# Kernel tuning notes

Measured on AMD Instinct MI355X. Metric: run time of the kernel, lower is better.

Reference implementation:

```python
import jax, jax.numpy as jnp
import numpy as np

B, DAYS, N, E = 2, 8, 10000, 80000
C_IN, C_OUT, H = 32, 32, 4
NEG_SLOPE = 0.2


def setup_inputs() -> dict:
    key = jax.random.key(0)
    ks = jax.random.split(key, 7)
    x = jax.random.randint(ks[0], (B, DAYS, N), 0, N)
    adjacency = jax.random.randint(ks[1], (2, E), 0, N)
    embedding = jax.random.normal(ks[2], (N, C_IN), dtype=jnp.float32)
    # GATConv linear: in_channels -> heads*out_channels
    W = jax.random.normal(ks[3], (C_IN, H * C_OUT), dtype=jnp.float32) / np.sqrt(C_IN)
    att_src = jax.random.normal(ks[4], (H, C_OUT), dtype=jnp.float32) / np.sqrt(C_OUT)
    att_dst = jax.random.normal(ks[5], (H, C_OUT), dtype=jnp.float32) / np.sqrt(C_OUT)
    bias = jnp.zeros((H * C_OUT,), dtype=jnp.float32)
    return {"x": x, "adjacency": adjacency, "embedding": embedding,
            "W": W, "att_src": att_src, "att_dst": att_dst, "bias": bias}


def _gat_forward(feat, src, dst, W, att_src, att_dst, bias):
    # feat: [G, N, C_IN]; same edge list shared across the G graphs
    G = feat.shape[0]
    xh = (feat @ W).reshape(G, N, H, C_OUT)              # [G,N,H,C]
    a_src = jnp.einsum('gnhc,hc->gnh', xh, att_src)       # [G,N,H]
    a_dst = jnp.einsum('gnhc,hc->gnh', xh, att_dst)
    alpha = a_src[:, src] + a_dst[:, dst]                 # [G,Et,H]
    alpha = jnp.where(alpha >= 0, alpha, NEG_SLOPE * alpha)

    def per_graph(al, msgs):
        # segment softmax over incoming edges of each dst node
        m = jax.ops.segment_max(al, dst, num_segments=N)  # [N,H]
        e = jnp.exp(al - m[dst])                          # [Et,H]
        s = jax.ops.segment_sum(e, dst, num_segments=N)
        w = e / (s[dst] + 1e-16)
        out = jax.ops.segment_sum(w[..., None] * msgs, dst, num_segments=N)
        return out                                        # [N,H,C]

    out = jax.vmap(per_graph)(alpha, xh[:, src])          # [G,N,H,C]
    return out.reshape(G, N, H * C_OUT) + bias


def reference(x, adjacency, embedding, W, att_src, att_dst, bias):
    Bd, Dd = x.shape[0], x.shape[1]
    feat = embedding[x].reshape(-1, N, C_IN)              # [G,N,C_IN]
    # GATConv default add_self_loops=True
    loops = jnp.arange(N, dtype=adjacency.dtype)
    src = jnp.concatenate([adjacency[0], loops])
    dst = jnp.concatenate([adjacency[1], loops])
    out = _gat_forward(feat, src, dst, W, att_src, att_dst, bias)
    return out.reshape(Bd, Dd, -1)
```

## Files before the change

### kernel.cpp

```cpp
#include <hip/hip_runtime.h>
#include <hip/hip_bf16.h>
#include <math.h>

#define C_IN 32
#define H 4
#define C_OUT 32
#define HC (H * C_OUT)
#define NEG_SLOPE 0.2f
#define CSR_STRIDE 64

typedef float v2f __attribute__((ext_vector_type(2)));

#define RPB 16
__global__ __launch_bounds__(256) void build_kernel(
        const int* __restrict__ adj, int E, int N,
        int* __restrict__ deg, int* __restrict__ csr,
        const float* __restrict__ emb, const float* __restrict__ W,
        const float* __restrict__ att_src, const float* __restrict__ att_dst,
        __hip_bfloat16* __restrict__ T, float* __restrict__ ta_src,
        float* __restrict__ ta_dst, int tblocks) {
    if ((int)blockIdx.x >= tblocks) {
        int e = (blockIdx.x - tblocks) * 256 + threadIdx.x;
        int Et = E + N;
        if (e < Et) {
            int s = (e < E) ? adj[e] : (e - E);
            int d = (e < E) ? adj[E + e] : (e - E);
            int pos = atomicAdd(&deg[d], 1);
            if (pos < CSR_STRIDE) csr[(d << 6) + pos] = s;
        }
        return;
    }
    int t = threadIdx.x;
    int sub = t >> 7;
    int tc = t & 127;
    int h = tc >> 5, c = tc & 31;
    int base = blockIdx.x * RPB;
    int nmax = (N - base < RPB) ? (N - base) : RPB;

    float wcol[C_IN];
#pragma unroll
    for (int k = 0; k < C_IN; k++) wcol[k] = W[k * HC + tc];
    float as = att_src[h * C_OUT + c];
    float adw = att_dst[h * C_OUT + c];

    for (int it = sub; it < nmax; it += 2) {
        int r = __builtin_amdgcn_readfirstlane(base + it);
        const float* ep = emb + (size_t)r * C_IN;
        float acc = 0.f;
#pragma unroll
        for (int k = 0; k < C_IN; k++) acc += ep[k] * wcol[k];
        T[(size_t)r * HC + tc] = __float2bfloat16(acc);
        float ps = acc * as, pd = acc * adw;
#pragma unroll
        for (int o = 16; o; o >>= 1) {
            ps += __shfl_xor(ps, o, 32);
            pd += __shfl_xor(pd, o, 32);
        }
        if (c == 0) {
            ta_src[r * H + h] = ps;
            ta_dst[r * H + h] = pd;
        }
    }
}

__global__ __launch_bounds__(256) void agg_kernel(
        const int* __restrict__ deg, const int* __restrict__ csr,
        const int* __restrict__ x, const uint2* __restrict__ Tu2,
        const float* __restrict__ ta_src, const float* __restrict__ ta_dst,
        const float* __restrict__ bias, float* __restrict__ out, int N, int G) {
    int wid = threadIdx.x >> 6;
    int lane = threadIdx.x & 63;
    int g = blockIdx.y * 4 + wid;
    if (g >= G) return;
    int n = blockIdx.x;

    int half = lane >> 5;
    int q = lane & 31;
    int hq = q >> 3;
    int h16 = lane >> 4;
    int e_sub = lane & 15;
    int widx = (hq << 4) + half;

    int dg = deg[n];
    if (dg > CSR_STRIDE) dg = CSR_STRIDE;
    int cbase = n << 6;
    const int* xg_arr = x + (size_t)g * N;
    int xgn = xg_arr[n];
    float ad = ta_dst[xgn * H + h16];

    float dsum = 0.f;
    v2f a01 = {0.f, 0.f}, a23 = {0.f, 0.f};

    for (int c0 = 0; c0 < dg; c0 += 16) {
        int cnt = dg - c0;
        cnt = (cnt > 16) ? 16 : cnt;
        int xg_e = 0;
        float w_pre = 0.f;
        if (e_sub < cnt) {
            int s = csr[cbase + c0 + e_sub];
            xg_e = xg_arr[s];
            float v = ta_src[xg_e * H + h16] + ad;
            v = (v >= 0.f) ? v : NEG_SLOPE * v;
            w_pre = __expf(v);
        }
        int ntrip = (cnt + 1) >> 1;
#pragma unroll
        for (int i = 0; i < 8; i++) {
            if (i >= ntrip) break;
            float w = __shfl(w_pre, widx + 2 * i, 64);
            int xg = __shfl(xg_e, half + 2 * i, 64);
            uint2 u = Tu2[(xg << 5) + q];
            v2f wv = {w, w};
            v2f t01 = {__uint_as_float(u.x << 16), __uint_as_float(u.x & 0xffff0000u)};
            v2f t23 = {__uint_as_float(u.y << 16), __uint_as_float(u.y & 0xffff0000u)};
            a01 += wv * t01;
            a23 += wv * t23;
            dsum += w;
        }
    }
    a01.x += __shfl_xor(a01.x, 32, 64);
    a01.y += __shfl_xor(a01.y, 32, 64);
    a23.x += __shfl_xor(a23.x, 32, 64);
    a23.y += __shfl_xor(a23.y, 32, 64);
    dsum  += __shfl_xor(dsum, 32, 64);
    float inv = 1.f / (dsum + 1e-16f);

    int cb = q * 4 + half * 2;
    float2 b2 = *(const float2*)(bias + cb);
    float2 o2;
    o2.x = (half ? a23.x : a01.x) * inv + b2.x;
    o2.y = (half ? a23.y : a01.y) * inv + b2.y;
    *(float2*)(out + ((size_t)g * N + n) * HC + cb) = o2;
}

extern "C" void kernel_launch(void* const* d_in, const int* in_sizes, int n_in,
                              void* d_out, int out_size, void* d_ws, size_t ws_size,
                              hipStream_t stream) {
    const int*   x       = (const int*)d_in[0];
    const int*   adj     = (const int*)d_in[1];
    const float* emb     = (const float*)d_in[2];
    const float* W       = (const float*)d_in[3];
    const float* att_src = (const float*)d_in[4];
    const float* att_dst = (const float*)d_in[5];
    const float* bias    = (const float*)d_in[6];
    float* out = (float*)d_out;

    const int N  = in_sizes[2] / C_IN;
    const int GN = in_sizes[0];
    const int G  = GN / N;
    const int E  = in_sizes[1] / 2;
    const int Et = E + N;

    char* ws = (char*)d_ws;
    size_t o = 0;
    auto carve = [&](size_t bytes) -> void* {
        void* p = ws + o;
        o = (o + bytes + 255) & ~(size_t)255;
        return p;
    };
    __hip_bfloat16* T = (__hip_bfloat16*)carve((size_t)N * HC * sizeof(__hip_bfloat16));
    float* ta_src  = (float*)carve((size_t)N * H * sizeof(float));
    float* ta_dst  = (float*)carve((size_t)N * H * sizeof(float));
    int*   deg     = (int*)carve((size_t)N * sizeof(int));
    int*   csr     = (int*)carve((size_t)N * CSR_STRIDE * sizeof(int));

    hipMemsetAsync(deg, 0, (size_t)N * sizeof(int), stream);

    int tblocks = (N + RPB - 1) / RPB;
    int fblocks = (Et + 255) / 256;
    build_kernel<<<tblocks + fblocks, 256, 0, stream>>>(
        adj, E, N, deg, csr, emb, W, att_src, att_dst, T, ta_src, ta_dst, tblocks);

    dim3 agrid(N, (G + 3) / 4);
    agg_kernel<<<agrid, 256, 0, stream>>>(deg, csr, x,
                                          (const uint2*)T, ta_src, ta_dst,
                                          bias, out, N, G);
}
```

Baseline: 178.0 us.

## Process all graphs per wave for one node, reusing CSR reads across graphs

The aggregation kernel now assigns one wavefront per destination node and handles all G graphs (up to 16) inside it, in place of one wave per (node, graph) pair. Each edge's source index is read once and shared across graphs. Lanes are remapped so that each lane computes the attention logit for one (graph, head) pair and then accumulates two output channels per graph. The aim is to amortise CSR and degree loads across graphs and shrink the grid. In exchange it uses 16 v2f accumulators per lane, which adds register pressure, and it silently assumes G <= 16.

```diff
diff --git a/kernel.cpp b/kernel.cpp
--- a/kernel.cpp
+++ b/kernel.cpp
@@ -8,6 +8,7 @@
 #define HC (H * C_OUT)
 #define NEG_SLOPE 0.2f
 #define CSR_STRIDE 64
+#define G_MAX 16
 
 typedef float v2f __attribute__((ext_vector_type(2)));
 
@@ -65,72 +66,74 @@
 
 __global__ __launch_bounds__(256) void agg_kernel(
         const int* __restrict__ deg, const int* __restrict__ csr,
-        const int* __restrict__ x, const uint2* __restrict__ Tu2,
+        const int* __restrict__ x, const unsigned int* __restrict__ Tu,
         const float* __restrict__ ta_src, const float* __restrict__ ta_dst,
         const float* __restrict__ bias, float* __restrict__ out, int N, int G) {
     int wid = threadIdx.x >> 6;
     int lane = threadIdx.x & 63;
-    int g = blockIdx.y * 4 + wid;
-    if (g >= G) return;
-    int n = blockIdx.x;
+    int n = blockIdx.x * 4 + wid;
+    if (n >= N) return;
 
-    int half = lane >> 5;
-    int q = lane & 31;
-    int hq = q >> 3;
-    int h16 = lane >> 4;
-    int e_sub = lane & 15;
-    int widx = (hq << 4) + half;
+    int g1 = lane >> 2;
+    int h1 = lane & 3;
+    int h2 = lane >> 4;
+    int gc1 = (g1 < G) ? g1 : (G - 1);
 
     int dg = deg[n];
     if (dg > CSR_STRIDE) dg = CSR_STRIDE;
-    int cbase = n << 6;
-    const int* xg_arr = x + (size_t)g * N;
-    int xgn = xg_arr[n];
-    float ad = ta_dst[xgn * H + h16];
+    const int* cb = csr + (n << 6);
 
-    float dsum = 0.f;
-    v2f a01 = {0.f, 0.f}, a23 = {0.f, 0.f};
+    int xgn = x[(size_t)gc1 * N + n];
+    float ad = ta_dst[xgn * H + h1];
 
-    for (int c0 = 0; c0 < dg; c0 += 16) {
+    v2f acc[G_MAX];
+    float dsum[G_MAX];
+#pragma unroll
+    for (int g = 0; g < G_MAX; g++) { acc[g] = (v2f){0.f, 0.f}; dsum[g] = 0.f; }
+
+    for (int c0 = 0; c0 < dg; c0 += 8) {
         int cnt = dg - c0;
-        cnt = (cnt > 16) ? 16 : cnt;
-        int xg_e = 0;
-        float w_pre = 0.f;
-        if (e_sub < cnt) {
-            int s = csr[cbase + c0 + e_sub];
-            xg_e = xg_arr[s];
-            float v = ta_src[xg_e * H + h16] + ad;
-            v = (v >= 0.f) ? v : NEG_SLOPE * v;
-            w_pre = __expf(v);
+        cnt = (cnt > 8) ? 8 : cnt;
+        float w_pre[8];
+        int xs_pre[8];
+#pragma unroll
+        for (int e = 0; e < 8; e++) {
+            w_pre[e] = 0.f;
+            xs_pre[e] = 0;
+            if (e < cnt) {
+                int s = __builtin_amdgcn_readfirstlane(cb[c0 + e]);
+                int xs = x[(size_t)gc1 * N + s];
+                xs_pre[e] = xs;
+                float a = ta_src[xs * H + h1] + ad;
+                a = (a >= 0.f) ? a : NEG_SLOPE * a;
+                w_pre[e] = __expf(a);
+            }
         }
-        int ntrip = (cnt + 1) >> 1;
 #pragma unroll
-        for (int i = 0; i < 8; i++) {
-            if (i >= ntrip) break;
-            float w = __shfl(w_pre, widx + 2 * i, 64);
-            int xg = __shfl(xg_e, half + 2 * i, 64);
-            uint2 u = Tu2[(xg << 5) + q];
-            v2f wv = {w, w};
-            v2f t01 = {__uint_as_float(u.x << 16), __uint_as_float(u.x & 0xffff0000u)};
-            v2f t23 = {__uint_as_float(u.y << 16), __uint_as_float(u.y & 0xffff0000u)};
-            a01 += wv * t01;
-            a23 += wv * t23;
-            dsum += w;
+        for (int e = 0; e < 8; e++) {
+            if (e >= cnt) break;
+#pragma unroll
+            for (int g = 0; g < G_MAX; g++) {
+                float w = __shfl(w_pre[e], g * 4 + h2, 64);
+                int xg = __builtin_amdgcn_readlane(xs_pre[e], g * 4);
+                unsigned int u = Tu[(xg << 6) + lane];
+                v2f t = {__uint_as_float(u << 16),
+                         __uint_as_float(u & 0xffff0000u)};
+                acc[g] += (v2f){w, w} * t;
+                dsum[g] += w;
+            }
         }
     }
-    a01.x += __shfl_xor(a01.x, 32, 64);
-    a01.y += __shfl_xor(a01.y, 32, 64);
-    a23.x += __shfl_xor(a23.x, 32, 64);
-    a23.y += __shfl_xor(a23.y, 32, 64);
-    dsum  += __shfl_xor(dsum, 32, 64);
-    float inv = 1.f / (dsum + 1e-16f);
 
-    int cb = q * 4 + half * 2;
-    float2 b2 = *(const float2*)(bias + cb);
-    float2 o2;
-    o2.x = (half ? a23.x : a01.x) * inv + b2.x;
-    o2.y = (half ? a23.y : a01.y) * inv + b2.y;
-    *(float2*)(out + ((size_t)g * N + n) * HC + cb) = o2;
+    float2 b2 = *(const float2*)(bias + lane * 2);
+    size_t obase = (size_t)n * HC + lane * 2;
+    for (int g = 0; g < G; g++) {
+        float inv = __builtin_amdgcn_rcpf(dsum[g] + 1e-16f);
+        float2 o2;
+        o2.x = acc[g].x * inv + b2.x;
+        o2.y = acc[g].y * inv + b2.y;
+        *(float2*)(out + obase + (size_t)g * N * HC) = o2;
+    }
 }
 
 extern "C" void kernel_launch(void* const* d_in, const int* in_sizes, int n_in,
@@ -171,8 +174,7 @@
     build_kernel<<<tblocks + fblocks, 256, 0, stream>>>(
         adj, E, N, deg, csr, emb, W, att_src, att_dst, T, ta_src, ta_dst, tblocks);
 
-    dim3 agrid(N, (G + 3) / 4);
-    agg_kernel<<<agrid, 256, 0, stream>>>(deg, csr, x,
-                                          (const uint2*)T, ta_src, ta_dst,
-                                          bias, out, N, G);
+    agg_kernel<<<(N + 3) / 4, 256, 0, stream>>>(deg, csr, x,
+                                                (const unsigned int*)T, ta_src, ta_dst,
+                                                bias, out, N, G);
 }
```

Measured after the change: 172.8 us. -2.9%, faster.
